# Kernel tuning notes

Measured on AMD Instinct MI355X. Metric: run time of the kernel, lower is better.

## Reference

```python
import jax, jax.numpy as jnp
import numpy as np

INPUT_SIZE = 1024
HIDDEN_SIZE = 2048
BATCH = 8192


def setup_inputs() -> dict:
    key = jax.random.key(0)
    k1, k2, k3, k4, k5 = jax.random.split(key, 5)
    input_tensor = jax.random.normal(k1, (BATCH, INPUT_SIZE), dtype=jnp.float32)
    h_0 = jax.random.normal(k2, (BATCH, HIDDEN_SIZE), dtype=jnp.float32)
    c_0 = jax.random.normal(k3, (BATCH, HIDDEN_SIZE), dtype=jnp.float32)
    # parameters: weight [input_size, 3*hidden], weight_hidden [hidden, 3*hidden], bias [3*hidden]
    weight = jax.random.normal(k4, (INPUT_SIZE, 3 * HIDDEN_SIZE), dtype=jnp.float32) * 0.02
    weight_hidden = jax.random.normal(k5, (HIDDEN_SIZE, 3 * HIDDEN_SIZE), dtype=jnp.float32) * 0.02
    bias = jnp.zeros((3 * HIDDEN_SIZE,), dtype=jnp.float32)
    return {
        "input_tensor": input_tensor,
        "h_0": h_0,
        "c_0": c_0,
        "weight": weight,
        "weight_hidden": weight_hidden,
        "bias": bias,
    }


def reference(input_tensor, h_0, c_0, weight, weight_hidden, bias):
    hidden_size = h_0.shape[-1]
    # pre-activations: x @ W + h_0 @ W_h + b  -> [batch, 3*hidden]
    gates = input_tensor @ weight + h_0 @ weight_hidden + bias
    f, i, c = jnp.split(gates, 3, axis=1)
    # c_1 = sigmoid(f) * c_0 + sigmoid(i) * tanh(c)
    c_1 = jax.nn.sigmoid(f) * c_0 + jax.nn.sigmoid(i) * jnp.tanh(c)
    return c_1
```

## Files before the change

### kernel.cpp

```cpp
#include <hip/hip_runtime.h>
#include <stdint.h>


#define BATCH 8192
#define INSZ  1024
#define HID   2048
#define NG    6144
#define KTOT  3072
#define KTILES 96

typedef __attribute__((ext_vector_type(8))) short short8;
typedef __attribute__((ext_vector_type(4))) short short4v;
typedef __attribute__((ext_vector_type(4))) float f32x4;
typedef __attribute__((ext_vector_type(4))) unsigned short u16x4;
typedef __attribute__((ext_vector_type(8))) unsigned short u16x8;

__device__ __forceinline__ unsigned short f32_to_bf16(float f) {
  uint32_t u = __builtin_bit_cast(uint32_t, f);
  u += 0x7fffu + ((u >> 16) & 1u);
  return (unsigned short)(u >> 16);
}


__global__ __launch_bounds__(256) void pack_a_kernel(
    const float* __restrict__ x, const float* __restrict__ h,
    unsigned short* __restrict__ Ap) {
  uint32_t q   = blockIdx.x * 256u + threadIdx.x;
  uint32_t kk4 = q & 7u;
  uint32_t m   = (q >> 3) & 8191u;
  uint32_t kt  = q >> 16;
  uint32_t k   = kt * 32u + kk4 * 4u;
  const float* src = (k < INSZ) ? (x + (size_t)m * INSZ + k)
                                : (h + (size_t)m * HID + (k - INSZ));
  float4 v = *(const float4*)src;
  u16x4 o;
  o.x = f32_to_bf16(v.x); o.y = f32_to_bf16(v.y);
  o.z = f32_to_bf16(v.z); o.w = f32_to_bf16(v.w);
  *(u16x4*)(Ap + ((size_t)kt * BATCH + m) * 32 + kk4 * 4) = o;
}

__global__ __launch_bounds__(256) void pack_b_kernel(
    const float* __restrict__ W, const float* __restrict__ Wh,
    unsigned short* __restrict__ Bp) {
  __shared__ unsigned short tile[128 * 34];
  const uint32_t kt = blockIdx.x / 48u;
  const uint32_t nt = blockIdx.x % 48u;
  const uint32_t k0 = kt * 32u, n0 = nt * 128u;
#pragma unroll
  for (int i = 0; i < 4; ++i) {
    uint32_t p  = i * 256u + threadIdx.x;
    uint32_t kk = p >> 5;
    uint32_t n4 = (p & 31u) * 4u;
    uint32_t k  = k0 + kk;
    const float* src = (k < INSZ) ? (W + (size_t)k * NG + n0 + n4)
                                  : (Wh + (size_t)(k - INSZ) * NG + n0 + n4);
    float4 v = *(const float4*)src;
    tile[(n4 + 0) * 34 + kk] = f32_to_bf16(v.x);
    tile[(n4 + 1) * 34 + kk] = f32_to_bf16(v.y);
    tile[(n4 + 2) * 34 + kk] = f32_to_bf16(v.z);
    tile[(n4 + 3) * 34 + kk] = f32_to_bf16(v.w);
  }
  __syncthreads();
#pragma unroll
  for (int i = 0; i < 2; ++i) {
    uint32_t p = i * 256u + threadIdx.x;
    uint32_t n = p >> 2, u = p & 3u;
    u16x8 val;
#pragma unroll
    for (int j = 0; j < 8; ++j) val[j] = tile[n * 34 + u * 8 + j];
    *(u16x8*)(Bp + ((size_t)kt * NG + n0 + n) * 32 + u * 8) = val;
  }
}

__device__ __forceinline__ void lstm_epilogue(
    const f32x4 acc[4][6], int m0, int j0, int wm, int wn, int quad, int l16,
    const float* __restrict__ bias, const float* __restrict__ c0,
    float* __restrict__ out) {
#pragma unroll
  for (int mi = 0; mi < 4; ++mi) {
    int rowb = m0 + wm * 64 + mi * 16 + quad * 4;
#pragma unroll
    for (int p = 0; p < 2; ++p) {
      int j = j0 + (2 * wn + p) * 16 + l16;
      float bfv = bias[j], biv = bias[HID + j], bcv = bias[2 * HID + j];
#pragma unroll
      for (int r = 0; r < 4; ++r) {
        size_t idx = (size_t)(rowb + r) * HID + j;
        float fg = acc[mi][0 + p][r] + bfv;
        float ig = acc[mi][2 + p][r] + biv;
        float cg = acc[mi][4 + p][r] + bcv;
        float sf = 1.f / (1.f + __expf(-fg));
        float si = 1.f / (1.f + __expf(-ig));
        float th = 2.f / (1.f + __expf(-2.f * cg)) - 1.f;
        out[idx] = sf * c0[idx] + si * th;
      }
    }
  }
}

__global__ __launch_bounds__(256) void gemm_packed_kernel(
    const unsigned short* __restrict__ Ap, const unsigned short* __restrict__ Bp,
    const float* __restrict__ bias, const float* __restrict__ c0,
    float* __restrict__ out) {
  __shared__ __align__(16) unsigned short As[128 * 32];
  __shared__ __align__(16) unsigned short Bs[192 * 32];
  const int tid = threadIdx.x;
  const int lane = tid & 63, w = tid >> 6;
  const int wm = w >> 1, wn = w & 1;
  const int quad = lane >> 4, l16 = lane & 15;
  const int bx = blockIdx.x;
  const int jt = bx & 31, mt = bx >> 5;
  const int m0 = mt * 128, j0 = jt * 64;

  f32x4 acc[4][6];
#pragma unroll
  for (int a = 0; a < 4; ++a)
#pragma unroll
    for (int b = 0; b < 6; ++b) acc[a][b] = (f32x4){0.f, 0.f, 0.f, 0.f};

  for (int kt = 0; kt < KTILES; ++kt) {
    const unsigned short* ga = Ap + ((size_t)kt * BATCH + m0) * 32;
#pragma unroll
    for (int i = 0; i < 2; ++i) {
      int t2 = w * 2 + i;
      __builtin_amdgcn_global_load_lds(
          (__attribute__((address_space(1))) void*)(void*)(ga + t2 * 512 + lane * 8),
          (__attribute__((address_space(3))) void*)(As + t2 * 512), 16, 0, 0);
    }
#pragma unroll
    for (int i = 0; i < 3; ++i) {
      int t = w * 3 + i;
      int g = t >> 2, sub = t & 3;
      const unsigned short* gb =
          Bp + ((size_t)kt * NG + g * HID + j0 + sub * 16) * 32;
      __builtin_amdgcn_global_load_lds(
          (__attribute__((address_space(1))) void*)(void*)(gb + lane * 8),
          (__attribute__((address_space(3))) void*)(Bs + t * 512), 16, 0, 0);
    }
    __syncthreads();
    short8 af[4], bf[6];
#pragma unroll
    for (int mi = 0; mi < 4; ++mi)
      af[mi] = *(const short8*)(As + (wm * 64 + mi * 16 + l16) * 32 + quad * 8);
#pragma unroll
    for (int g = 0; g < 3; ++g)
#pragma unroll
      for (int p = 0; p < 2; ++p)
        bf[g * 2 + p] = *(const short8*)(
            Bs + (g * 64 + (2 * wn + p) * 16 + l16) * 32 + quad * 8);
#pragma unroll
    for (int mi = 0; mi < 4; ++mi)
#pragma unroll
      for (int f = 0; f < 6; ++f)
        acc[mi][f] =
            __builtin_amdgcn_mfma_f32_16x16x32_bf16(af[mi], bf[f], acc[mi][f], 0, 0, 0);
    __syncthreads();
  }
  lstm_epilogue(acc, m0, j0, wm, wn, quad, l16, bias, c0, out);
}

__global__ __launch_bounds__(256) void gemm_f32_kernel(
    const float* __restrict__ x, const float* __restrict__ h,
    const float* __restrict__ W, const float* __restrict__ Wh,
    const float* __restrict__ bias, const float* __restrict__ c0,
    float* __restrict__ out) {
  __shared__ __align__(16) unsigned short As[128 * 36];
  __shared__ __align__(16) unsigned short Bs[192 * 36];
  const int tid = threadIdx.x;
  const int lane = tid & 63, w = tid >> 6;
  const int wm = w >> 1, wn = w & 1;
  const int quad = lane >> 4, l16 = lane & 15;
  const int bx = blockIdx.x;
  const int jt = bx & 31, mt = bx >> 5;
  const int m0 = mt * 128, j0 = jt * 64;

  f32x4 acc[4][6];
#pragma unroll
  for (int a = 0; a < 4; ++a)
#pragma unroll
    for (int b = 0; b < 6; ++b) acc[a][b] = (f32x4){0.f, 0.f, 0.f, 0.f};

  for (int kt = 0; kt < KTILES; ++kt) {
    int k0 = kt * 32;
#pragma unroll
    for (int i = 0; i < 4; ++i) {
      int q = i * 256 + tid;
      int m = q >> 3, kk = (q & 7) * 4;
      int k = k0 + kk;
      const float* src = (k < INSZ) ? (x + (size_t)(m0 + m) * INSZ + k)
                                    : (h + (size_t)(m0 + m) * HID + (k - INSZ));
      float4 v = *(const float4*)src;
      u16x4 o;
      o.x = f32_to_bf16(v.x); o.y = f32_to_bf16(v.y);
      o.z = f32_to_bf16(v.z); o.w = f32_to_bf16(v.w);
      *(u16x4*)(As + m * 36 + kk) = o;
    }
#pragma unroll
    for (int i = 0; i < 6; ++i) {
      int q = i * 256 + tid;
      int n = q % 192, kq = (q / 192) * 4;
      int col = (n >> 6) * HID + j0 + (n & 63);
      float vv[4];
#pragma unroll
      for (int t = 0; t < 4; ++t) {
        int k = k0 + kq + t;
        vv[t] = (k < INSZ) ? W[(size_t)k * NG + col]
                           : Wh[(size_t)(k - INSZ) * NG + col];
      }
      u16x4 o;
      o.x = f32_to_bf16(vv[0]); o.y = f32_to_bf16(vv[1]);
      o.z = f32_to_bf16(vv[2]); o.w = f32_to_bf16(vv[3]);
      *(u16x4*)(Bs + n * 36 + kq) = o;
    }
    __syncthreads();
    short8 af[4], bf[6];
#pragma unroll
    for (int mi = 0; mi < 4; ++mi) {
      int base = (wm * 64 + mi * 16 + l16) * 36 + quad * 8;
      short4v lo = *(const short4v*)(As + base);
      short4v hi = *(const short4v*)(As + base + 4);
      af[mi] = __builtin_shufflevector(lo, hi, 0, 1, 2, 3, 4, 5, 6, 7);
    }
#pragma unroll
    for (int g = 0; g < 3; ++g)
#pragma unroll
      for (int p = 0; p < 2; ++p) {
        int base = (g * 64 + (2 * wn + p) * 16 + l16) * 36 + quad * 8;
        short4v lo = *(const short4v*)(Bs + base);
        short4v hi = *(const short4v*)(Bs + base + 4);
        bf[g * 2 + p] = __builtin_shufflevector(lo, hi, 0, 1, 2, 3, 4, 5, 6, 7);
      }
#pragma unroll
    for (int mi = 0; mi < 4; ++mi)
#pragma unroll
      for (int f = 0; f < 6; ++f)
        acc[mi][f] =
            __builtin_amdgcn_mfma_f32_16x16x32_bf16(af[mi], bf[f], acc[mi][f], 0, 0, 0);
    __syncthreads();
  }
  lstm_epilogue(acc, m0, j0, wm, wn, quad, l16, bias, c0, out);
}

extern "C" void kernel_launch(void* const* d_in, const int* in_sizes, int n_in,
                              void* d_out, int out_size, void* d_ws, size_t ws_size,
                              hipStream_t stream) {
  const float* x    = (const float*)d_in[0];
  const float* h0   = (const float*)d_in[1];
  const float* c0   = (const float*)d_in[2];
  const float* W    = (const float*)d_in[3];
  const float* Wh   = (const float*)d_in[4];
  const float* bias = (const float*)d_in[5];
  float* out = (float*)d_out;

  const size_t needA = (size_t)KTOT * BATCH * 2;
  const size_t needB = (size_t)KTOT * NG * 2;
  if (ws_size >= needA + needB) {
    unsigned short* Ap = (unsigned short*)d_ws;
    unsigned short* Bp = Ap + (size_t)KTOT * BATCH;
    pack_a_kernel<<<24576, 256, 0, stream>>>(x, h0, Ap);
    pack_b_kernel<<<4608, 256, 0, stream>>>(W, Wh, Bp);
    gemm_packed_kernel<<<2048, 256, 0, stream>>>(Ap, Bp, bias, c0, out);
  } else {
    gemm_f32_kernel<<<2048, 256, 0, stream>>>(x, h0, W, Wh, bias, c0, out);
  }
}
```

Before: 665.5 us.

## Load B fragments directly to registers with prefetch, swizzle A in LDS

The GEMM no longer stages B through shared memory. Each wave loads its B fragments straight from global memory into registers, double-buffered one k-tile ahead. The A pack writes a XOR-swizzled layout so that A fragment reads from LDS avoid bank conflicts. The block ordering is flipped so consecutive blocks share the same B column tile, and the B pack kernel is rewritten as a simple per-thread gather without an LDS transpose. The trade-offs are higher register pressure, B reads that are no longer shared across the waves of a block (wm pairs read the same B), and a B pack whose global reads are strided by k.

```diff
diff --git a/kernel.cpp b/kernel.cpp
--- a/kernel.cpp
+++ b/kernel.cpp
@@ -13,7 +13,6 @@
 typedef __attribute__((ext_vector_type(4))) short short4v;
 typedef __attribute__((ext_vector_type(4))) float f32x4;
 typedef __attribute__((ext_vector_type(4))) unsigned short u16x4;
-typedef __attribute__((ext_vector_type(8))) unsigned short u16x8;
 
 __device__ __forceinline__ unsigned short f32_to_bf16(float f) {
   uint32_t u = __builtin_bit_cast(uint32_t, f);
@@ -36,40 +35,31 @@
   u16x4 o;
   o.x = f32_to_bf16(v.x); o.y = f32_to_bf16(v.y);
   o.z = f32_to_bf16(v.z); o.w = f32_to_bf16(v.w);
-  *(u16x4*)(Ap + ((size_t)kt * BATCH + m) * 32 + kk4 * 4) = o;
+  uint32_t c  = kk4 >> 1, hh = kk4 & 1;
+  uint32_t sm = (m + (m >> 2)) & 3u;
+  *(u16x4*)(Ap + ((size_t)kt * BATCH + m) * 32 + ((c ^ sm) * 8 + hh * 4)) = o;
 }
 
 __global__ __launch_bounds__(256) void pack_b_kernel(
     const float* __restrict__ W, const float* __restrict__ Wh,
     unsigned short* __restrict__ Bp) {
-  __shared__ unsigned short tile[128 * 34];
-  const uint32_t kt = blockIdx.x / 48u;
-  const uint32_t nt = blockIdx.x % 48u;
-  const uint32_t k0 = kt * 32u, n0 = nt * 128u;
-#pragma unroll
-  for (int i = 0; i < 4; ++i) {
-    uint32_t p  = i * 256u + threadIdx.x;
-    uint32_t kk = p >> 5;
-    uint32_t n4 = (p & 31u) * 4u;
-    uint32_t k  = k0 + kk;
-    const float* src = (k < INSZ) ? (W + (size_t)k * NG + n0 + n4)
-                                  : (Wh + (size_t)(k - INSZ) * NG + n0 + n4);
-    float4 v = *(const float4*)src;
-    tile[(n4 + 0) * 34 + kk] = f32_to_bf16(v.x);
-    tile[(n4 + 1) * 34 + kk] = f32_to_bf16(v.y);
-    tile[(n4 + 2) * 34 + kk] = f32_to_bf16(v.z);
-    tile[(n4 + 3) * 34 + kk] = f32_to_bf16(v.w);
-  }
-  __syncthreads();
-#pragma unroll
-  for (int i = 0; i < 2; ++i) {
-    uint32_t p = i * 256u + threadIdx.x;
-    uint32_t n = p >> 2, u = p & 3u;
-    u16x8 val;
-#pragma unroll
-    for (int j = 0; j < 8; ++j) val[j] = tile[n * 34 + u * 8 + j];
-    *(u16x8*)(Bp + ((size_t)kt * NG + n0 + n) * 32 + u * 8) = val;
-  }
+  uint32_t q  = blockIdx.x * 256u + threadIdx.x;
+  uint32_t hh = q & 7u;
+  uint32_t r  = q >> 3;
+  uint32_t n  = r % 6144u;
+  uint32_t kt = r / 6144u;
+  uint32_t k0 = kt * 32u + hh * 4u;
+  float v[4];
+#pragma unroll
+  for (int t = 0; t < 4; ++t) {
+    uint32_t k = k0 + t;
+    v[t] = (k < INSZ) ? W[(size_t)k * NG + n]
+                      : Wh[(size_t)(k - INSZ) * NG + n];
+  }
+  u16x4 o;
+  o.x = f32_to_bf16(v[0]); o.y = f32_to_bf16(v[1]);
+  o.z = f32_to_bf16(v[2]); o.w = f32_to_bf16(v[3]);
+  *(u16x4*)(Bp + ((size_t)kt * NG + n) * 32 + hh * 4) = o;
 }
 
 __device__ __forceinline__ void lstm_epilogue(
@@ -103,14 +93,14 @@
     const float* __restrict__ bias, const float* __restrict__ c0,
     float* __restrict__ out) {
   __shared__ __align__(16) unsigned short As[128 * 32];
-  __shared__ __align__(16) unsigned short Bs[192 * 32];
   const int tid = threadIdx.x;
   const int lane = tid & 63, w = tid >> 6;
   const int wm = w >> 1, wn = w & 1;
   const int quad = lane >> 4, l16 = lane & 15;
   const int bx = blockIdx.x;
-  const int jt = bx & 31, mt = bx >> 5;
+  const int mt = bx & 63, jt = bx >> 6;
   const int m0 = mt * 128, j0 = jt * 64;
+  const int sw = (l16 + (l16 >> 2)) & 3;
 
   f32x4 acc[4][6];
 #pragma unroll
@@ -118,7 +108,19 @@
 #pragma unroll
     for (int b = 0; b < 6; ++b) acc[a][b] = (f32x4){0.f, 0.f, 0.f, 0.f};
 
+  const unsigned short* bb =
+      Bp + ((size_t)(j0 + 2 * wn * 16 + l16)) * 32 + quad * 8;
+
+  short8 bf[2][6];
+#pragma unroll
+  for (int g = 0; g < 3; ++g)
+#pragma unroll
+    for (int p = 0; p < 2; ++p)
+      bf[0][g * 2 + p] = *(const short8*)(bb + g * (HID * 32) + p * 512);
+
+#pragma unroll 2
   for (int kt = 0; kt < KTILES; ++kt) {
+    const int cur = kt & 1;
     const unsigned short* ga = Ap + ((size_t)kt * BATCH + m0) * 32;
 #pragma unroll
     for (int i = 0; i < 2; ++i) {
@@ -127,33 +129,26 @@
           (__attribute__((address_space(1))) void*)(void*)(ga + t2 * 512 + lane * 8),
           (__attribute__((address_space(3))) void*)(As + t2 * 512), 16, 0, 0);
     }
-#pragma unroll
-    for (int i = 0; i < 3; ++i) {
-      int t = w * 3 + i;
-      int g = t >> 2, sub = t & 3;
-      const unsigned short* gb =
-          Bp + ((size_t)kt * NG + g * HID + j0 + sub * 16) * 32;
-      __builtin_amdgcn_global_load_lds(
-          (__attribute__((address_space(1))) void*)(void*)(gb + lane * 8),
-          (__attribute__((address_space(3))) void*)(Bs + t * 512), 16, 0, 0);
-    }
-    __syncthreads();
-    short8 af[4], bf[6];
+    __syncthreads();
+    if (kt + 1 < KTILES) {
+      const unsigned short* bn = bb + (size_t)(kt + 1) * (NG * 32);
+#pragma unroll
+      for (int g = 0; g < 3; ++g)
+#pragma unroll
+        for (int p = 0; p < 2; ++p)
+          bf[cur ^ 1][g * 2 + p] = *(const short8*)(bn + g * (HID * 32) + p * 512);
+    }
+    short8 af[4];
 #pragma unroll
     for (int mi = 0; mi < 4; ++mi)
-      af[mi] = *(const short8*)(As + (wm * 64 + mi * 16 + l16) * 32 + quad * 8);
-#pragma unroll
-    for (int g = 0; g < 3; ++g)
-#pragma unroll
-      for (int p = 0; p < 2; ++p)
-        bf[g * 2 + p] = *(const short8*)(
-            Bs + (g * 64 + (2 * wn + p) * 16 + l16) * 32 + quad * 8);
+      af[mi] = *(const short8*)(
+          As + (wm * 64 + mi * 16 + l16) * 32 + ((quad ^ sw) * 8));
 #pragma unroll
     for (int mi = 0; mi < 4; ++mi)
 #pragma unroll
       for (int f = 0; f < 6; ++f)
         acc[mi][f] =
-            __builtin_amdgcn_mfma_f32_16x16x32_bf16(af[mi], bf[f], acc[mi][f], 0, 0, 0);
+            __builtin_amdgcn_mfma_f32_16x16x32_bf16(af[mi], bf[cur][f], acc[mi][f], 0, 0, 0);
     __syncthreads();
   }
   lstm_epilogue(acc, m0, j0, wm, wn, quad, l16, bias, c0, out);
@@ -258,7 +253,7 @@
     unsigned short* Ap = (unsigned short*)d_ws;
     unsigned short* Bp = Ap + (size_t)KTOT * BATCH;
     pack_a_kernel<<<24576, 256, 0, stream>>>(x, h0, Ap);
-    pack_b_kernel<<<4608, 256, 0, stream>>>(W, Wh, Bp);
+    pack_b_kernel<<<18432, 256, 0, stream>>>(W, Wh, Bp);
     gemm_packed_kernel<<<2048, 256, 0, stream>>>(Ap, Bp, bias, c0, out);
   } else {
     gemm_f32_kernel<<<2048, 256, 0, stream>>>(x, h0, W, Wh, bias, c0, out);
```

Result: faster. 636.0 us (-4.4%).
